# Performance work log

Hardware: AMD Instinct MI355X
Metric: run time of the kernel (lower is better)

## Reference

```python
import math
import jax, jax.numpy as jnp
import numpy as np

B, N, F_IN, F_H, F_OUT = 8, 2048, 128, 256, 256
RATIOS = (0.8, 0.5)
EDGE_P = 0.01  # adjacency density -> avg degree ~20


def setup_inputs() -> dict:
    key = jax.random.key(0)
    kx, ka, k1, k2, k3, k4, k5, k6 = jax.random.split(key, 8)
    x = jax.random.normal(kx, (B, N, F_IN), dtype=jnp.float32)
    u = jax.random.uniform(ka, (B, N, N), dtype=jnp.float32)
    # sparse nonneg weighted adjacency, zero diagonal (so gcn self-loop add == A + I)
    A = jnp.where(u < EDGE_P, u / EDGE_P, 0.0) * (1.0 - jnp.eye(N, dtype=jnp.float32))
    s_in, s_h = 1.0 / math.sqrt(F_IN), 1.0 / math.sqrt(F_H)
    W1 = jax.random.normal(k1, (F_IN, F_H), dtype=jnp.float32) * s_in
    b1 = jnp.zeros((F_H,), dtype=jnp.float32)
    p1 = jax.random.normal(k2, (F_H,), dtype=jnp.float32) * s_h
    W2 = jax.random.normal(k3, (F_H, F_OUT), dtype=jnp.float32) * s_h
    b2 = jnp.zeros((F_OUT,), dtype=jnp.float32)
    p2 = jax.random.normal(k4, (F_OUT,), dtype=jnp.float32) * s_h
    return {"x": x, "A": A, "W1": W1, "b1": b1, "p1": p1, "W2": W2, "b2": b2, "p2": p2}


def _gcn(x, A, W, b):
    # PyG GCNConv with gcn_norm: A_hat = A + I (diag(A)==0), deg = in-degree (col sums),
    # out[i] = sum_j dinv[j] * A_hat[j, i] * dinv[i] * (xW)[j] + b
    n = A.shape[0]
    A_hat = A + jnp.eye(n, dtype=A.dtype)
    dinv = jax.lax.rsqrt(A_hat.sum(axis=0))  # deg >= 1 due to self loops
    M = dinv[:, None] * A_hat * dinv[None, :]
    return M.T @ (x @ W) + b


def _topk_pool(x, A, p, k):
    # score = tanh(x @ p / ||p||); keep top-k nodes, scale features by score
    score = jnp.tanh((x @ p) / jnp.linalg.norm(p))
    vals, perm = jax.lax.top_k(score, k)
    return x[perm] * vals[:, None], A[perm][:, perm]


def _per_graph(x0, A0, W1, b1, p1, W2, b2, p2):
    n = x0.shape[0]
    k1 = math.ceil(RATIOS[0] * n)
    k2 = math.ceil(RATIOS[1] * k1)
    h = jax.nn.relu(_gcn(x0, A0, W1, b1))          # dropout is identity in eval mode
    h, A1 = _topk_pool(h, A0, p1, k1)
    h = jax.nn.relu(_gcn(h, A1, W2, b2))
    h, _ = _topk_pool(h, A1, p2, k2)
    # node_mask in the source is always all-True, so mean-fill never triggers:
    # rows [:k2] = pooled features, rest zeros.
    return jnp.zeros((n, h.shape[1]), dtype=h.dtype).at[:k2].set(h)


def reference(x, A, W1, b1, p1, W2, b2, p2):
    f = lambda xi, Ai: _per_graph(xi, Ai, W1, b1, p1, W2, b2, p2)
    return jax.vmap(f)(x, A)  # [B, N, F_OUT]
```

## Files before the change

kernel.cpp:

```cpp
#include <hip/hip_runtime.h>
#include <math.h>

#define BATCH 8
#define NN    2048
#define FIN   128
#define FH    256
#define KP1   1639
#define KP2   820
#define CAP   64

__global__ __launch_bounds__(256) void init_all(int* __restrict__ cnt,
                                                int* __restrict__ inv,
                                                const float* __restrict__ p1,
                                                const float* __restrict__ p2,
                                                double* __restrict__ norms) {
  int t = blockIdx.x * 256 + threadIdx.x;
  if (t < BATCH * NN) { cnt[t] = 0; inv[t] = -1; }
  if (blockIdx.x == 0) {
    __shared__ double red[256];
    int f = threadIdx.x;
    double v = (double)p1[f];
    red[f] = v * v;
    __syncthreads();
    for (int s = 128; s > 0; s >>= 1) { if (f < s) red[f] += red[f + s]; __syncthreads(); }
    if (f == 0) norms[0] = sqrt(red[0]);
    __syncthreads();
    v = (double)p2[f];
    red[f] = v * v;
    __syncthreads();
    for (int s = 128; s > 0; s >>= 1) { if (f < s) red[f] += red[f + s]; __syncthreads(); }
    if (f == 0) norms[1] = sqrt(red[0]);
  }
}

__global__ void build_csc1(const float* __restrict__ A, int* __restrict__ cnt,
                           int* __restrict__ idx, float* __restrict__ val) {
  const int total = BATCH * NN * (NN / 4);
  for (int t = blockIdx.x * blockDim.x + threadIdx.x; t < total;
       t += gridDim.x * blockDim.x) {
    float4 v4 = reinterpret_cast<const float4*>(A)[t];
    int b = t / (NN * NN / 4);
    int rem = t % (NN * NN / 4);
    int j = rem / (NN / 4);
    int i0 = (rem % (NN / 4)) * 4;
    float vv[4] = {v4.x, v4.y, v4.z, v4.w};
#pragma unroll
    for (int c = 0; c < 4; ++c) {
      float v = vv[c];
      if (v != 0.0f) {
        int col = b * NN + i0 + c;
        int p = atomicAdd(&cnt[col], 1);
        if (p < CAP) { idx[col * CAP + p] = j; val[col * CAP + p] = v; }
      }
    }
  }
}

__global__ __launch_bounds__(256) void canon_cols(int* __restrict__ cnt,
                                                  int* __restrict__ idx,
                                                  float* __restrict__ val,
                                                  double* __restrict__ dinv) {
  int wid = (blockIdx.x * blockDim.x + threadIdx.x) >> 6;
  int lane = threadIdx.x & 63;
  if (wid >= BATCH * NN) return;
  int c = cnt[wid]; if (c > CAP) c = CAP;
  if (lane == 0) cnt[wid] = c;
  int key = 0x7fffffff;
  float v = 0.0f;
  if (lane < c) {
    key = idx[(size_t)wid * CAP + lane];
    v = val[(size_t)wid * CAP + lane];
  }
#pragma unroll
  for (int k = 2; k <= 64; k <<= 1) {
#pragma unroll
    for (int j = k >> 1; j > 0; j >>= 1) {
      int pk = __shfl_xor(key, j);
      float pv = __shfl_xor(v, j);
      bool up = ((lane & k) == 0);
      bool takeMin = (((lane & j) == 0) == up);
      bool sw = takeMin ? (pk < key) : (pk > key);
      if (sw) { key = pk; v = pv; }
    }
  }
  if (lane < c) {
    idx[(size_t)wid * CAP + lane] = key;
    val[(size_t)wid * CAP + lane] = v;
  }
  double dv = (double)v;
#pragma unroll
  for (int off = 32; off > 0; off >>= 1) dv += __shfl_xor(dv, off);
  if (lane == 0) dinv[wid] = 1.0 / sqrt(1.0 + dv);
}

template <int KD, typename TX, bool GATHER>
__global__ __launch_bounds__(512) void gemm_y(const TX* __restrict__ X,
                                              const float* __restrict__ W,
                                              const double* __restrict__ dinv,
                                              double* __restrict__ Y, int rows,
                                              const int* __restrict__ perm,
                                              const double* __restrict__ gvals) {
  const int KC = 32;
  int bid = blockIdx.x;
  int b = bid & 7;
  int r0 = (bid >> 3) * 32;
  int t = threadIdx.x;
  int fq = (t & 63) * 4;
  int rg = (t >> 6) * 4;
  __shared__ TX xs[32][KC];
  __shared__ float wsh[KC][FH];
  const TX* Xb = X + (size_t)b * NN * KD;
  double acc[4][4];
#pragma unroll
  for (int r = 0; r < 4; ++r)
#pragma unroll
    for (int c = 0; c < 4; ++c) acc[r][c] = 0.0;

  for (int kc = 0; kc < KD; kc += KC) {
    __syncthreads();
    for (int e = t; e < 32 * KC; e += 512) {
      int r = e >> 5, k = e & 31;
      int row = r0 + r;
      if (GATHER) {
        if (row < rows) {
          int src = perm[b * NN + row];
          double scl = gvals[b * NN + row];
          xs[r][k] = (TX)(X[((size_t)b * NN + src) * KD + kc + k] * scl);
        } else {
          xs[r][k] = (TX)0;
        }
      } else {
        xs[r][k] = (row < rows) ? Xb[(size_t)row * KD + kc + k] : (TX)0;
      }
    }
    for (int e = t; e < KC * FH / 4; e += 512) {
      int k = e >> 6;
      int f = (e << 2) & 255;
      *reinterpret_cast<float4*>(&wsh[k][f]) =
          *reinterpret_cast<const float4*>(&W[(size_t)(kc + k) * FH + f]);
    }
    __syncthreads();
#pragma unroll 2
    for (int k = 0; k < KC; k += 2) {
      float4 waf = *reinterpret_cast<const float4*>(&wsh[k][fq]);
      float4 wbf = *reinterpret_cast<const float4*>(&wsh[k + 1][fq]);
      double wa0 = (double)waf.x, wa1 = (double)waf.y;
      double wa2 = (double)waf.z, wa3 = (double)waf.w;
      double wb0 = (double)wbf.x, wb1 = (double)wbf.y;
      double wb2 = (double)wbf.z, wb3 = (double)wbf.w;
#pragma unroll
      for (int r = 0; r < 4; ++r) {
        double x0 = (double)xs[rg + r][k];
        double x1 = (double)xs[rg + r][k + 1];
        acc[r][0] = fma(x1, wb0, fma(x0, wa0, acc[r][0]));
        acc[r][1] = fma(x1, wb1, fma(x0, wa1, acc[r][1]));
        acc[r][2] = fma(x1, wb2, fma(x0, wa2, acc[r][2]));
        acc[r][3] = fma(x1, wb3, fma(x0, wa3, acc[r][3]));
      }
    }
  }
#pragma unroll
  for (int r = 0; r < 4; ++r) {
    int row = r0 + rg + r;
    if (row < rows) {
      double d = dinv[b * NN + row];
      double* o = Y + ((size_t)b * NN + row) * FH + fq;
      o[0] = d * acc[r][0];
      o[1] = d * acc[r][1];
      o[2] = d * acc[r][2];
      o[3] = d * acc[r][3];
    }
  }
}

__global__ __launch_bounds__(FH) void aggregate(
    const double* __restrict__ Y, const int* __restrict__ cnt,
    const int* __restrict__ idx, const float* __restrict__ val,
    const double* __restrict__ dinv, const float* __restrict__ bias,
    const float* __restrict__ p, double* __restrict__ H, double* __restrict__ dot) {
  int b = blockIdx.x & 7, i = blockIdx.x >> 3, f = threadIdx.x;
  int col = b * NN + i;
  const int* ji = idx + (size_t)col * CAP;
  const float* jv = val + (size_t)col * CAP;
  const double* Yb = Y + (size_t)b * NN * FH;
  double acc = Y[(size_t)col * FH + f];
  int c = cnt[col];
  int a = 0;
  for (; a + 8 <= c; a += 8) {
    double tt[8];
    double vv[8];
#pragma unroll
    for (int u = 0; u < 8; ++u) {
      vv[u] = (double)jv[a + u];
      tt[u] = Yb[(size_t)ji[a + u] * FH + f];
    }
#pragma unroll
    for (int u = 0; u < 8; ++u) acc += vv[u] * tt[u];
  }
  for (; a < c; ++a) {
    acc += (double)jv[a] * Yb[(size_t)ji[a] * FH + f];
  }
  double h = fmax(dinv[col] * acc + (double)bias[f], 0.0);
  H[(size_t)col * FH + f] = h;
  double pd = h * (double)p[f];
#pragma unroll
  for (int off = 32; off > 0; off >>= 1) pd += __shfl_xor(pd, off);
  __shared__ double red[4];
  if ((f & 63) == 0) red[f >> 6] = pd;
  __syncthreads();
  if (f == 0) dot[col] = (red[0] + red[1]) + (red[2] + red[3]);
}

__global__ __launch_bounds__(1024) void topk_sort(
    const double* __restrict__ dot, const double* __restrict__ norms, int which,
    int valid, int k, int* __restrict__ perm, double* __restrict__ vals,
    int* __restrict__ inv) {
  __shared__ double sk[NN];
  __shared__ int si[NN];
  int b = blockIdx.x, t = threadIdx.x;
  double nrm = norms[which];
  for (int e = t; e < NN; e += 1024) {
    sk[e] = (e < valid) ? tanh(dot[b * NN + e] / nrm) : -1.0e300;
    si[e] = e;
  }
  for (int kk = 2; kk <= NN; kk <<= 1) {
    for (int j = kk >> 1; j > 0; j >>= 1) {
      __syncthreads();
      int i = ((t & ~(j - 1)) << 1) | (t & (j - 1));
      int q = i | j;
      double ka = sk[i], kb = sk[q];
      int ia = si[i], ib = si[q];
      bool p_first = (kb > ka) || (kb == ka && ib < ia);
      bool up = ((i & kk) == 0);
      if (up ? p_first : !p_first) { sk[i] = kb; sk[q] = ka; si[i] = ib; si[q] = ia; }
    }
  }
  __syncthreads();
  for (int e = t; e < k; e += 1024) {
    int node = si[e];
    perm[b * NN + e] = node;
    vals[b * NN + e] = sk[e];
    inv[b * NN + node] = e;
  }
}

__global__ __launch_bounds__(256) void build_csc2(
    const int* __restrict__ cnt1, const int* __restrict__ idx1,
    const float* __restrict__ val1, const int* __restrict__ perm,
    const int* __restrict__ inv, int* __restrict__ cnt2, int* __restrict__ idx2,
    float* __restrict__ val2, double* __restrict__ dinv2) {
  int wid = (blockIdx.x * blockDim.x + threadIdx.x) >> 6;
  int lane = threadIdx.x & 63;
  if (wid >= BATCH * KP1) return;
  int b = wid / KP1, ri = wid % KP1;
  int colA = b * NN + perm[b * NN + ri];
  int c = cnt1[colA];
  int rj = -1;
  float v = 0.0f;
  if (lane < c) {
    int j = idx1[(size_t)colA * CAP + lane];
    v = val1[(size_t)colA * CAP + lane];
    rj = inv[b * NN + j];
  }
  bool keep = (lane < c) && (rj >= 0);
  unsigned long long mask = __ballot(keep);
  int pos = __popcll(mask & ((1ull << lane) - 1ull));
  int colB = b * NN + ri;
  if (keep) {
    idx2[(size_t)colB * CAP + pos] = rj;
    val2[(size_t)colB * CAP + pos] = v;
  }
  if (lane == 0) cnt2[colB] = (int)__popcll(mask);
  double dv = keep ? (double)v : 0.0;
#pragma unroll
  for (int off = 32; off > 0; off >>= 1) dv += __shfl_xor(dv, off);
  if (lane == 0) dinv2[colB] = 1.0 / sqrt(1.0 + dv);
}

__global__ __launch_bounds__(FH) void final_kernel(
    const double* __restrict__ H2, const int* __restrict__ perm2,
    const double* __restrict__ vals2, float* __restrict__ out) {
  int b = blockIdx.x & 7, r = blockIdx.x >> 3, f = threadIdx.x;
  float o = 0.0f;
  if (r < KP2) {
    int rr = perm2[b * NN + r];
    o = (float)(H2[((size_t)b * NN + rr) * FH + f] * vals2[b * NN + r]);
  }
  out[((size_t)b * NN + r) * FH + f] = o;
}

extern "C" void kernel_launch(void* const* d_in, const int* in_sizes, int n_in,
                              void* d_out, int out_size, void* d_ws, size_t ws_size,
                              hipStream_t stream) {
  const float* x  = (const float*)d_in[0];
  const float* A  = (const float*)d_in[1];
  const float* W1 = (const float*)d_in[2];
  const float* b1 = (const float*)d_in[3];
  const float* p1 = (const float*)d_in[4];
  const float* W2 = (const float*)d_in[5];
  const float* b2 = (const float*)d_in[6];
  const float* p2 = (const float*)d_in[7];
  float* out = (float*)d_out;

  char* ws = (char*)d_ws;
  size_t off = 0;
  auto alloc = [&](size_t bytes) {
    void* p = ws + off;
    off += (bytes + 255) & ~(size_t)255;
    return p;
  };
  double* dot   = (double*)alloc((size_t)BATCH * NN * 8);
  double* y     = (double*)alloc((size_t)BATCH * NN * FH * 8);
  double* h     = (double*)alloc((size_t)BATCH * NN * FH * 8);
  double* dinv1 = (double*)alloc((size_t)BATCH * NN * 8);
  double* dinv2 = (double*)alloc((size_t)BATCH * NN * 8);
  int*   cnt1  = (int*)alloc((size_t)BATCH * NN * 4);
  int*   idx1  = (int*)alloc((size_t)BATCH * NN * CAP * 4);
  float* val1  = (float*)alloc((size_t)BATCH * NN * CAP * 4);
  int*   cnt2  = (int*)alloc((size_t)BATCH * NN * 4);
  int*   idx2  = (int*)alloc((size_t)BATCH * NN * CAP * 4);
  float* val2  = (float*)alloc((size_t)BATCH * NN * CAP * 4);
  int*   perm1 = (int*)alloc((size_t)BATCH * NN * 4);
  double* vals1 = (double*)alloc((size_t)BATCH * NN * 8);
  int*   perm2 = (int*)alloc((size_t)BATCH * NN * 4);
  double* vals2 = (double*)alloc((size_t)BATCH * NN * 8);
  int*   inv   = (int*)alloc((size_t)BATCH * NN * 4);
  double* norms = (double*)alloc(64);

  init_all<<<BATCH * NN / 256, 256, 0, stream>>>(cnt1, inv, p1, p2, norms);
  build_csc1<<<4096, 256, 0, stream>>>(A, cnt1, idx1, val1);
  canon_cols<<<(BATCH * NN * 64) / 256, 256, 0, stream>>>(cnt1, idx1, val1, dinv1);
  gemm_y<FIN, float, false><<<(NN / 32) * BATCH, 512, 0, stream>>>(
      x, W1, dinv1, y, NN, nullptr, nullptr);
  aggregate<<<NN * BATCH, FH, 0, stream>>>(y, cnt1, idx1, val1, dinv1, b1, p1, h, dot);
  topk_sort<<<BATCH, 1024, 0, stream>>>(dot, norms, 0, NN, KP1, perm1, vals1, inv);
  build_csc2<<<(BATCH * KP1 * 64 + 255) / 256, 256, 0, stream>>>(cnt1, idx1, val1, perm1,
                                                                 inv, cnt2, idx2, val2, dinv2);
  gemm_y<FH, double, true><<<((KP1 + 31) / 32) * BATCH, 512, 0, stream>>>(
      h, W2, dinv2, y, KP1, perm1, vals1);
  aggregate<<<KP1 * BATCH, FH, 0, stream>>>(y, cnt2, idx2, val2, dinv2, b2, p2, h, dot);
  topk_sort<<<BATCH, 1024, 0, stream>>>(dot, norms, 1, KP1, KP2, perm2, vals2, inv);
  final_kernel<<<NN * BATCH, FH, 0, stream>>>(h, perm2, vals2, out);
}
```

Before: 298.9 us.

## Replace single-block bitonic top-k sort with parallel rank-counting kernel

The per-graph bitonic sort, run as one 1024-thread block per graph with many barrier stages, is replaced by a rank kernel in which each thread counts how many scores beat its own. Work is spread over many blocks per graph, and the tanh is applied only to kept elements. Ranking on raw dot products assumes tanh/norm preserves order, and the comparison work grows quadratically.

New measurement: 358.0 us. 1.2x slower.

```diff
diff --git a/kernel.cpp b/kernel.cpp
--- a/kernel.cpp
+++ b/kernel.cpp
@@ -211,36 +211,31 @@
   if (f == 0) dot[col] = (red[0] + red[1]) + (red[2] + red[3]);
 }
 
-__global__ __launch_bounds__(1024) void topk_sort(
+__global__ __launch_bounds__(256) void topk_rank(
     const double* __restrict__ dot, const double* __restrict__ norms, int which,
-    int valid, int k, int* __restrict__ perm, double* __restrict__ vals,
+    int valid, int kk, int* __restrict__ perm, double* __restrict__ vals,
     int* __restrict__ inv) {
-  __shared__ double sk[NN];
-  __shared__ int si[NN];
-  int b = blockIdx.x, t = threadIdx.x;
-  double nrm = norms[which];
-  for (int e = t; e < NN; e += 1024) {
-    sk[e] = (e < valid) ? tanh(dot[b * NN + e] / nrm) : -1.0e300;
-    si[e] = e;
-  }
-  for (int kk = 2; kk <= NN; kk <<= 1) {
-    for (int j = kk >> 1; j > 0; j >>= 1) {
-      __syncthreads();
-      int i = ((t & ~(j - 1)) << 1) | (t & (j - 1));
-      int q = i | j;
-      double ka = sk[i], kb = sk[q];
-      int ia = si[i], ib = si[q];
-      bool p_first = (kb > ka) || (kb == ka && ib < ia);
-      bool up = ((i & kk) == 0);
-      if (up ? p_first : !p_first) { sk[i] = kb; sk[q] = ka; si[i] = ib; si[q] = ia; }
-    }
-  }
+  __shared__ double kd[NN];
+  int b = blockIdx.y, t = threadIdx.x;
+  for (int e = t; e < valid; e += 256) kd[e] = dot[b * NN + e];
   __syncthreads();
-  for (int e = t; e < k; e += 1024) {
-    int node = si[e];
-    perm[b * NN + e] = node;
-    vals[b * NN + e] = sk[e];
-    inv[b * NN + node] = e;
+  int e = blockIdx.x * 256 + t;
+  if (e >= valid) return;
+  double de = kd[e];
+  int rank = 0;
+  int j = 0;
+  for (; j + 4 <= valid; j += 4) {
+    double k0 = kd[j], k1 = kd[j + 1], k2 = kd[j + 2], k3 = kd[j + 3];
+    rank += (k0 > de) || (k0 == de && (j + 0) < e);
+    rank += (k1 > de) || (k1 == de && (j + 1) < e);
+    rank += (k2 > de) || (k2 == de && (j + 2) < e);
+    rank += (k3 > de) || (k3 == de && (j + 3) < e);
+  }
+  for (; j < valid; ++j) rank += (kd[j] > de) || (kd[j] == de && j < e);
+  if (rank < kk) {
+    perm[b * NN + rank] = e;
+    vals[b * NN + rank] = tanh(de / norms[which]);
+    inv[b * NN + e] = rank;
   }
 }
 
@@ -333,12 +328,14 @@
   gemm_y<FIN, float, false><<<(NN / 32) * BATCH, 512, 0, stream>>>(
       x, W1, dinv1, y, NN, nullptr, nullptr);
   aggregate<<<NN * BATCH, FH, 0, stream>>>(y, cnt1, idx1, val1, dinv1, b1, p1, h, dot);
-  topk_sort<<<BATCH, 1024, 0, stream>>>(dot, norms, 0, NN, KP1, perm1, vals1, inv);
+  topk_rank<<<dim3(NN / 256, BATCH), 256, 0, stream>>>(dot, norms, 0, NN, KP1,
+                                                       perm1, vals1, inv);
   build_csc2<<<(BATCH * KP1 * 64 + 255) / 256, 256, 0, stream>>>(cnt1, idx1, val1, perm1,
                                                                  inv, cnt2, idx2, val2, dinv2);
   gemm_y<FH, double, true><<<((KP1 + 31) / 32) * BATCH, 512, 0, stream>>>(
       h, W2, dinv2, y, KP1, perm1, vals1);
   aggregate<<<KP1 * BATCH, FH, 0, stream>>>(y, cnt2, idx2, val2, dinv2, b2, p2, h, dot);
-  topk_sort<<<BATCH, 1024, 0, stream>>>(dot, norms, 1, KP1, KP2, perm2, vals2, inv);
+  topk_rank<<<dim3((KP1 + 255) / 256, BATCH), 256, 0, stream>>>(dot, norms, 1, KP1, KP2,
+                                                                perm2, vals2, inv);
   final_kernel<<<NN * BATCH, FH, 0, stream>>>(h, perm2, vals2, out);
 }
```
